# Kernel tuning notes

Hardware: AMD Instinct MI355X
Metric: run time of the kernel (lower is better)

The kernel has to match this reference:

```python
import jax, jax.numpy as jnp
import numpy as np

N = 50000   # nodes
E = 800000  # edges (avg degree 16)
G = 64      # graphs in batch

def _lin(k, fi, fo):
    kw, kb = jax.random.split(k)
    s = 1.0 / np.sqrt(fi)
    w = jax.random.uniform(kw, (fi, fo), minval=-s, maxval=s, dtype=jnp.float32)
    b = jax.random.uniform(kb, (fo,), minval=-s, maxval=s, dtype=jnp.float32)
    return w, b

def setup_inputs():
    key = jax.random.key(0)
    ks = jax.random.split(key, 12)
    pos = jax.random.normal(ks[0], (N, 3), dtype=jnp.float32)
    edge_index = jax.random.randint(ks[1], (2, E), 0, N, dtype=jnp.int32)
    batch = jnp.sort(jax.random.randint(ks[2], (N,), 0, G, dtype=jnp.int32))
    w_proj, b_proj = _lin(ks[3], 3, 64)
    # message passing layers: self-weight, neighbor-weight, bias
    ws0, bb0 = _lin(ks[4], 64, 64);  wn0, _ = _lin(jax.random.fold_in(ks[4], 1), 64, 64)
    ws1, bb1 = _lin(ks[5], 64, 64);  wn1, _ = _lin(jax.random.fold_in(ks[5], 1), 64, 64)
    ws2, bb2 = _lin(ks[6], 64, 128); wn2, _ = _lin(jax.random.fold_in(ks[6], 1), 64, 128)
    ws3, bb3 = _lin(ks[7], 256, 256); wn3, _ = _lin(jax.random.fold_in(ks[7], 1), 256, 256)
    # dense head: concat(max, mean) = 512 -> 512 -> 256
    wd1, bd1 = _lin(ks[8], 512, 512)
    wd2, bd2 = _lin(ks[9], 512, 256)
    return {"pos": pos, "edge_index": edge_index, "batch": batch,
            "w_proj": w_proj, "b_proj": b_proj,
            "ws0": ws0, "wn0": wn0, "bb0": bb0,
            "ws1": ws1, "wn1": wn1, "bb1": bb1,
            "ws2": ws2, "wn2": wn2, "bb2": bb2,
            "ws3": ws3, "wn3": wn3, "bb3": bb3,
            "wd1": wd1, "bd1": bd1, "wd2": wd2, "bd2": bd2}

def reference(pos, edge_index, batch, w_proj, b_proj,
              ws0, wn0, bb0, ws1, wn1, bb1, ws2, wn2, bb2, ws3, wn3, bb3,
              wd1, bd1, wd2, bd2):
    src, dst = edge_index[0], edge_index[1]
    x = pos @ w_proj + b_proj  # node projection [N,64]
    # in-degree counts, computed once
    deg = jnp.maximum(
        jax.ops.segment_sum(jnp.ones((E, 1), x.dtype), dst, num_segments=N), 1.0)

    def mp(h, ws, wn, b):
        # mean-aggregate neighbor messages: gather on src, scatter-add on dst
        agg = jax.ops.segment_sum(h[src], dst, num_segments=N) / deg
        return jax.nn.leaky_relu(h @ ws + agg @ wn + b)

    h0 = mp(x, ws0, wn0, bb0)   # [N,64]
    h1 = mp(h0, ws1, wn1, bb1)  # [N,64]
    h2 = mp(h1, ws2, wn2, bb2)  # [N,128]
    nf = mp(jnp.concatenate([h0, h1, h2], axis=-1), ws3, wn3, bb3)  # [N,256]

    # scatter max/mean pooling over graph ids
    gcnt = jnp.maximum(
        jax.ops.segment_sum(jnp.ones((N, 1), nf.dtype), batch, num_segments=G), 1.0)
    x1 = jax.ops.segment_max(nf, batch, num_segments=G)
    x2 = jax.ops.segment_sum(nf, batch, num_segments=G) / gcnt
    g = jnp.concatenate([x1, x2], axis=-1)  # [G,512]

    g = jax.nn.leaky_relu(g @ wd1 + bd1)
    return g @ wd2 + bd2  # [G,256]
```

## Files before the change

### kernel.cpp

```cpp
#include <hip/hip_runtime.h>
#include <math.h>

typedef _Float16 f16x8 __attribute__((ext_vector_type(8)));
typedef unsigned short us8 __attribute__((ext_vector_type(8)));
typedef float f32x4 __attribute__((ext_vector_type(4)));

__device__ inline unsigned short f2h(float f) {
    _Float16 h = (_Float16)f;
    return *(unsigned short*)&h;
}
__device__ inline float h2f(unsigned short u) {
    _Float16 h = *(_Float16*)&u;
    return (float)h;
}

__device__ __forceinline__ size_t pkoff(int row, int col, int KT) {
    return ((size_t)(row >> 4) * (KT >> 5) + (col >> 5)) * 512
         + (size_t)(((col >> 3) & 3) * 128 + ((row & 15) << 3) + (col & 7));
}

#define ECH 4096

__global__ __launch_bounds__(256)
void bucket_hist(const int* __restrict__ edst, int* __restrict__ bcnt, int E, int NB) {
    __shared__ int h[512];
    int tid = threadIdx.x;
    for (int i = tid; i < NB; i += 256) h[i] = 0;
    __syncthreads();
    int c0 = blockIdx.x * ECH, c1 = min(c0 + ECH, E);
    for (int e = c0 + tid; e < c1; e += 256) atomicAdd(&h[edst[e] >> 7], 1);
    __syncthreads();
    for (int i = tid; i < NB; i += 256) if (h[i]) atomicAdd(&bcnt[i], h[i]);
}

__global__ __launch_bounds__(512)
void bucket_scan(const int* __restrict__ bcnt, int* __restrict__ bbase,
                 int* __restrict__ bcur, int* __restrict__ rowstart, int NB, int n) {
    __shared__ int ws[8];
    int tid = threadIdx.x, lane = tid & 63, wid = tid >> 6;
    int v = (tid < NB) ? bcnt[tid] : 0;
    int x = v;
    for (int d = 1; d < 64; d <<= 1) { int y = __shfl_up(x, d); if (lane >= d) x += y; }
    if (lane == 63) ws[wid] = x;
    __syncthreads();
    int off = 0;
    for (int w = 0; w < wid; w++) off += ws[w];
    int excl = x - v + off;
    if (tid < NB) { bbase[tid] = excl; bcur[tid] = excl; }
    if (tid == 0) {
        int tot = 0;
        for (int w = 0; w < 8; w++) tot += ws[w];
        bbase[NB] = tot;
        rowstart[n] = tot;
    }
}

__global__ __launch_bounds__(256)
void bucket_scatter(const int* __restrict__ esrc_in, const int* __restrict__ edst_in,
                    int* __restrict__ bcur, unsigned* __restrict__ bedge, int E, int NB) {
    __shared__ int h[512];
    __shared__ int rb[512];
    int tid = threadIdx.x;
    for (int i = tid; i < NB; i += 256) h[i] = 0;
    __syncthreads();
    int c0 = blockIdx.x * ECH, c1 = min(c0 + ECH, E);
    for (int e = c0 + tid; e < c1; e += 256) atomicAdd(&h[edst_in[e] >> 7], 1);
    __syncthreads();
    for (int i = tid; i < NB; i += 256) {
        rb[i] = h[i] ? atomicAdd(&bcur[i], h[i]) : 0;
        h[i] = 0;
    }
    __syncthreads();
    for (int e = c0 + tid; e < c1; e += 256) {
        int dst = edst_in[e], src = esrc_in[e];
        int b = dst >> 7;
        int o = atomicAdd(&h[b], 1);
        bedge[rb[b] + o] = (unsigned)src | ((unsigned)(dst & 127) << 16);
    }
}

__global__ __launch_bounds__(256)
void node_csr(const unsigned* __restrict__ bedge, const int* __restrict__ bbase,
              int* __restrict__ rowstart, float* __restrict__ degf,
              unsigned short* __restrict__ esrc, int n) {
    __shared__ int cnt[128];
    __shared__ int cur[128];
    __shared__ int ws4[4];
    int b = blockIdx.x, tid = threadIdx.x;
    int lane = tid & 63, wid = tid >> 6;
    int n0 = b << 7;
    int eb0 = bbase[b], eb1 = bbase[b + 1];
    if (tid < 128) cnt[tid] = 0;
    __syncthreads();
    for (int e = eb0 + tid; e < eb1; e += 256) atomicAdd(&cnt[(bedge[e] >> 16) & 127], 1);
    __syncthreads();
    int v = (tid < 128) ? cnt[tid] : 0;
    int x = v;
    for (int d = 1; d < 64; d <<= 1) { int y = __shfl_up(x, d); if (lane >= d) x += y; }
    if (lane == 63) ws4[wid] = x;
    __syncthreads();
    int off = 0;
    for (int w = 0; w < wid; w++) off += ws4[w];
    int excl = x - v + off;
    if (tid < 128 && n0 + tid < n) {
        rowstart[n0 + tid] = eb0 + excl;
        cur[tid] = eb0 + excl;
        degf[n0 + tid] = (float)(v > 0 ? v : 1);
    }
    __syncthreads();
    for (int e = eb0 + tid; e < eb1; e += 256) {
        unsigned u = bedge[e];
        int p = atomicAdd(&cur[(u >> 16) & 127], 1);
        esrc[p] = (unsigned short)(u & 0xffffu);
    }
}

__global__ __launch_bounds__(256)
void prep_k(int* __restrict__ bcnt, float* __restrict__ pmax, float* __restrict__ psum, int G,
            const float* __restrict__ ws1, const float* __restrict__ wn1, unsigned short* __restrict__ WP1,
            const float* __restrict__ ws2, const float* __restrict__ wn2, unsigned short* __restrict__ WP2,
            const float* __restrict__ ws3, const float* __restrict__ wn3, unsigned short* __restrict__ WP3,
            const float* __restrict__ wp, const float* __restrict__ bp,
            const float* __restrict__ ws0, const float* __restrict__ wn0, const float* __restrict__ bb0,
            float* __restrict__ W0c, float* __restrict__ b0c,
            const float* __restrict__ pos, unsigned short* __restrict__ pos16, int N) {
    int t = blockIdx.x * 256 + threadIdx.x;
    if (t < 512) bcnt[t] = 0;
    if (t < G * 256) { pmax[t] = -INFINITY; psum[t] = 0.f; }
    if (t < 8192) {
        int k = t >> 6, n = t & 63;
        float v = (k < 64) ? ws1[k * 64 + n] : wn1[(k - 64) * 64 + n];
        WP1[pkoff(n, k, 128)] = f2h(v);
    }
    if (t < 16384) {
        int k = t >> 7, n = t & 127;
        float v = (k < 64) ? ws2[k * 128 + n] : wn2[(k - 64) * 128 + n];
        WP2[pkoff(n, k, 128)] = f2h(v);
    }
    if (t < 131072) {
        int k = t >> 8, n = t & 255;
        float v = (k < 256) ? ws3[k * 256 + n] : wn3[(k - 256) * 256 + n];
        WP3[pkoff(n, k, 512)] = f2h(v);
    }
    if (t < 384) {
        int j = t / 64, f = t & 63;
        const float* W = (j < 3) ? ws0 : wn0;
        int jj = (j < 3) ? j : j - 3;
        float acc = 0.f;
        for (int c = 0; c < 64; c++) acc += wp[jj * 64 + c] * W[c * 64 + f];
        W0c[j * 64 + f] = acc;
    }
    if (t < 64) {
        float acc = bb0[t];
        for (int c = 0; c < 64; c++) acc += bp[c] * (ws0[c * 64 + t] + wn0[c * 64 + t]);
        b0c[t] = acc;
    }
    if (t < 4 * N) {
        int n = t >> 2, j = t & 3;
        pos16[t] = (j < 3) ? f2h(pos[n * 3 + j]) : 0;
    }
}

__global__ __launch_bounds__(256)
void l0_k(const float* __restrict__ pos, const unsigned short* __restrict__ pos16,
          const float* __restrict__ W0c, const float* __restrict__ b0c,
          const int* __restrict__ rowstart, const unsigned short* __restrict__ esrc,
          const float* __restrict__ degf,
          unsigned short* __restrict__ XBrow, unsigned short* __restrict__ XBpk, int n_nodes) {
    int wave = threadIdx.x >> 6, lane = threadIdx.x & 63;
    int n = blockIdx.x * 4 + wave;
    if (n >= n_nodes) return;
    int e0 = rowstart[n], e1 = rowstart[n + 1];
    float ax = 0.f, ay = 0.f, az = 0.f;
    for (int e = e0 + lane; e < e1; e += 64) {
        int s = esrc[e];
        uint2 q = *(const uint2*)&pos16[(size_t)s * 4];
        ax += h2f((unsigned short)(q.x & 0xffffu));
        ay += h2f((unsigned short)(q.x >> 16));
        az += h2f((unsigned short)(q.y & 0xffffu));
    }
    #pragma unroll
    for (int d = 32; d; d >>= 1) {
        ax += __shfl_xor(ax, d);
        ay += __shfl_xor(ay, d);
        az += __shfl_xor(az, d);
    }
    float inv = 1.0f / degf[n];
    ax *= inv; ay *= inv; az *= inv;
    float px = pos[n * 3 + 0], py = pos[n * 3 + 1], pz = pos[n * 3 + 2];
    int f = lane;
    float v = b0c[f] + px * W0c[f] + py * W0c[64 + f] + pz * W0c[128 + f]
            + ax * W0c[192 + f] + ay * W0c[256 + f] + az * W0c[320 + f];
    v = (v > 0.f) ? v : 0.01f * v;
    unsigned short h = f2h(v);
    XBrow[(size_t)n * 256 + f] = h;
    XBpk[pkoff(n, f, 512)] = h;
}

template <int F, int KT>
__global__ __launch_bounds__(256)
void agg_pk(const unsigned short* __restrict__ src, int sstr,
            unsigned short* __restrict__ dpk, int dc,
            const int* __restrict__ rowstart, const unsigned short* __restrict__ esrc,
            const float* __restrict__ degf, int n_nodes) {
    int wave = threadIdx.x >> 6;
    int lane = threadIdx.x & 63;
    int n = blockIdx.x * 4 + wave;
    if (n >= n_nodes) return;
    const int ST = (F == 64) ? 2 : 1;
    int half = (F == 64) ? (lane >> 5) : 0;
    int li   = (F == 64) ? (lane & 31) : lane;
    int e0 = rowstart[n], e1 = rowstart[n + 1];
    float a0 = 0.f, a1 = 0.f;
    int e = e0 + half;
    for (; e + 7 * ST < e1; e += 8 * ST) {
        int s[8];
        unsigned p[8];
        #pragma unroll
        for (int j = 0; j < 8; j++) s[j] = esrc[e + j * ST];
        #pragma unroll
        for (int j = 0; j < 8; j++) p[j] = *(const unsigned*)&src[(size_t)s[j] * sstr + 2 * li];
        #pragma unroll
        for (int j = 0; j < 8; j++) {
            a0 += h2f((unsigned short)(p[j] & 0xffffu));
            a1 += h2f((unsigned short)(p[j] >> 16));
        }
    }
    for (; e + 3 * ST < e1; e += 4 * ST) {
        int s[4];
        unsigned p[4];
        #pragma unroll
        for (int j = 0; j < 4; j++) s[j] = esrc[e + j * ST];
        #pragma unroll
        for (int j = 0; j < 4; j++) p[j] = *(const unsigned*)&src[(size_t)s[j] * sstr + 2 * li];
        #pragma unroll
        for (int j = 0; j < 4; j++) {
            a0 += h2f((unsigned short)(p[j] & 0xffffu));
            a1 += h2f((unsigned short)(p[j] >> 16));
        }
    }
    for (; e < e1; e += ST) {
        int s = esrc[e];
        unsigned p = *(const unsigned*)&src[(size_t)s * sstr + 2 * li];
        a0 += h2f((unsigned short)(p & 0xffffu));
        a1 += h2f((unsigned short)(p >> 16));
    }
    if (F == 64) { a0 += __shfl_xor(a0, 32); a1 += __shfl_xor(a1, 32); }
    float inv = 1.0f / degf[n];
    unsigned out = (unsigned)f2h(a0 * inv) | ((unsigned)f2h(a1 * inv) << 16);
    if (F != 64 || lane < 32) {
        int c = dc + 2 * li;
        *(unsigned*)&dpk[pkoff(n, c, KT)] = out;
    }
}

__device__ inline void atomicMaxFloat(float* addr, float v) {
    if (v >= 0.f) atomicMax((int*)addr, __float_as_int(v));
    else          atomicMin((unsigned int*)addr, __float_as_uint(v));
}

template <int K, int KTA, int MT, int NTB, int POOL>
__global__ __launch_bounds__(256)
void gemm_fr(const unsigned short* __restrict__ Apk, int KA1, int ac1, int ac2,
             const unsigned short* __restrict__ Wpk, const float* __restrict__ bias,
             unsigned short* __restrict__ Drow, int dcol,
             unsigned short* __restrict__ Dpk, int KTD,
             float* __restrict__ pmax, float* __restrict__ psum,
             const int* __restrict__ batch, int M) {
    const int NS = K / 32;
    const int TROW = NTB * 16 + 8;
    const int TSZ = POOL ? 4 : (MT * 16) * TROW;
    __shared__ unsigned short tile_s[4][TSZ];
    int w = threadIdx.x >> 6;
    int lane = threadIdx.x & 63;
    int lm = lane & 15, kb = lane >> 4;
    int rb0 = (blockIdx.x * 4 + w) * MT;
    int nb0 = blockIdx.y * NTB;
    int m0 = rb0 * 16;
    if (m0 >= M) return;
    unsigned short* tile = tile_s[w];

    f32x4 acc[MT][NTB] = {};

    auto loadf = [&](f16x8* A_, f16x8* B_, int s) {
        int kk = s * 32;
        int phys = (kk < KA1) ? (ac1 + kk) : (ac2 + (kk - KA1));
        size_t ak = (size_t)(phys >> 5) * 512 + (size_t)lane * 8;
        #pragma unroll
        for (int mf = 0; mf < MT; mf++)
            A_[mf] = *(const f16x8*)&Apk[(size_t)(rb0 + mf) * (KTA / 32) * 512 + ak];
        #pragma unroll
        for (int nt = 0; nt < NTB; nt++)
            B_[nt] = *(const f16x8*)&Wpk[((size_t)(nb0 + nt) * (K / 32) + s) * 512 + (size_t)lane * 8];
    };
    auto domfma = [&](f16x8* A_, f16x8* B_) {
        #pragma unroll
        for (int nt = 0; nt < NTB; nt++)
            #pragma unroll
            for (int mf = 0; mf < MT; mf++)
                acc[mf][nt] = __builtin_amdgcn_mfma_f32_16x16x32_f16(A_[mf], B_[nt], acc[mf][nt], 0, 0, 0);
    };

    f16x8 aA[MT], bA[NTB], aB[MT], bB[NTB];
    loadf(aA, bA, 0);
    for (int s = 0; s < NS; s += 2) {
        loadf(aB, bB, s + 1);
        domfma(aA, bA);
        if (s + 2 < NS) loadf(aA, bA, s + 2);
        domfma(aB, bB);
    }

    if (!POOL) {
        #pragma unroll
        for (int nt = 0; nt < NTB; nt++) {
            int colL = nt * 16 + lm;
            float bv = bias[nb0 * 16 + colL];
            #pragma unroll
            for (int mf = 0; mf < MT; mf++) {
                #pragma unroll
                for (int r = 0; r < 4; r++) {
                    float v = acc[mf][nt][r] + bv;
                    v = (v > 0.f) ? v : 0.01f * v;
                    unsigned short h = f2h(v);
                    tile[(mf * 16 + kb * 4 + r) * TROW + colL] = h;
                    int gm = m0 + mf * 16 + kb * 4 + r;
                    if (gm < M) Drow[(size_t)gm * 256 + dcol + nb0 * 16 + colL] = h;
                }
            }
        }
        int dkg0 = (dcol + nb0 * 16) >> 5;
        #pragma unroll
        for (int mf = 0; mf < MT; mf++) {
            #pragma unroll
            for (int kg = 0; kg < NTB / 2; kg++) {
                us8 u = *(const us8*)&tile[(mf * 16 + lm) * TROW + kg * 32 + kb * 8];
                *(us8*)&Dpk[((size_t)(rb0 + mf) * (KTD / 32) + dkg0 + kg) * 512 + (size_t)lane * 8] = u;
            }
        }
    } else {
        int grow[MT * 4];
        #pragma unroll
        for (int mf = 0; mf < MT; mf++)
            #pragma unroll
            for (int r = 0; r < 4; r++) {
                int gm = m0 + mf * 16 + kb * 4 + r;
                grow[mf * 4 + r] = batch[gm < M ? gm : (M - 1)];
            }
        int mlast = m0 + MT * 16 - 1;
        bool uni = (batch[m0] == batch[mlast < M ? mlast : (M - 1)]);
        if (uni) {
            int g = grow[0];
            #pragma unroll
            for (int nt = 0; nt < NTB; nt++) {
                int col = (nb0 + nt) * 16 + lm;
                float bv = bias[col];
                float mx = -INFINITY, sm = 0.f;
                #pragma unroll
                for (int mf = 0; mf < MT; mf++) {
                    #pragma unroll
                    for (int r = 0; r < 4; r++) {
                        int gm = m0 + mf * 16 + kb * 4 + r;
                        if (gm >= M) continue;
                        float v = acc[mf][nt][r] + bv;
                        v = (v > 0.f) ? v : 0.01f * v;
                        mx = fmaxf(mx, v); sm += v;
                    }
                }
                mx = fmaxf(mx, __shfl_xor(mx, 16));
                mx = fmaxf(mx, __shfl_xor(mx, 32));
                sm += __shfl_xor(sm, 16);
                sm += __shfl_xor(sm, 32);
                if (kb == 0 && mx > -INFINITY) {
                    atomicMaxFloat(&pmax[g * 256 + col], mx);
                    atomicAdd(&psum[g * 256 + col], sm);
                }
            }
        } else {
            #pragma unroll
            for (int nt = 0; nt < NTB; nt++) {
                int col = (nb0 + nt) * 16 + lm;
                float bv = bias[col];
                int curg = -1; float mx = -INFINITY, sm = 0.f;
                #pragma unroll
                for (int mf = 0; mf < MT; mf++) {
                    #pragma unroll
                    for (int r = 0; r < 4; r++) {
                        int gm = m0 + mf * 16 + kb * 4 + r;
                        if (gm >= M) continue;
                        int g = grow[mf * 4 + r];
                        if (g != curg) {
                            if (curg >= 0) {
                                atomicMaxFloat(&pmax[curg * 256 + col], mx);
                                atomicAdd(&psum[curg * 256 + col], sm);
                            }
                            curg = g; mx = -INFINITY; sm = 0.f;
                        }
                        float v = acc[mf][nt][r] + bv;
                        v = (v > 0.f) ? v : 0.01f * v;
                        mx = fmaxf(mx, v); sm += v;
                    }
                }
                if (curg >= 0) {
                    atomicMaxFloat(&pmax[curg * 256 + col], mx);
                    atomicAdd(&psum[curg * 256 + col], sm);
                }
            }
        }
    }
}

template <int K, int FOUT>
__global__ __launch_bounds__(256)
void gemm_lrelu(const float* __restrict__ A1, int a1s, int a1c, int KA1,
                const float* __restrict__ A2, int a2s, int a2c,
                const float* __restrict__ W1, const float* __restrict__ W2,
                const float* __restrict__ bias,
                float* __restrict__ D, int dstr, int dcol, int M, int doRelu) {
    const int BM = 64, BN = 64, BK = 16;
    __shared__ float As[BK][BM];
    __shared__ float Bs[BK][BN];
    int tid = threadIdx.x;
    int m0 = blockIdx.x * BM;
    int n0 = blockIdx.y * BN;
    int tx = tid & 15;
    int ty = tid >> 4;
    float acc[4][4] = {};
    int mA = tid >> 2;
    int kA = (tid & 3) * 4;
    int kB = tid >> 4;
    int nB = (tid & 15) * 4;
    for (int k0 = 0; k0 < K; k0 += BK) {
        int kk = k0 + kA;
        const float* Ap; int Asr; int Acc;
        if (kk < KA1) { Ap = A1; Asr = a1s; Acc = a1c + kk; }
        else          { Ap = A2; Asr = a2s; Acc = a2c + (kk - KA1); }
        int gm = m0 + mA;
        float4 av;
        if (gm < M) av = *(const float4*)&Ap[(size_t)gm * Asr + Acc];
        else        av = float4{0.f, 0.f, 0.f, 0.f};
        As[kA + 0][mA] = av.x; As[kA + 1][mA] = av.y;
        As[kA + 2][mA] = av.z; As[kA + 3][mA] = av.w;
        int kw = k0 + kB;
        const float* Wp; int kwl;
        if (kw < K / 2) { Wp = W1; kwl = kw; } else { Wp = W2; kwl = kw - K / 2; }
        float4 bv = *(const float4*)&Wp[(size_t)kwl * FOUT + n0 + nB];
        *(float4*)&Bs[kB][nB] = bv;
        __syncthreads();
        #pragma unroll
        for (int k = 0; k < BK; k++) {
            float a[4], b[4];
            *(float4*)a = *(const float4*)&As[k][ty * 4];
            *(float4*)b = *(const float4*)&Bs[k][tx * 4];
            #pragma unroll
            for (int i = 0; i < 4; i++)
                #pragma unroll
                for (int j = 0; j < 4; j++)
                    acc[i][j] += a[i] * b[j];
        }
        __syncthreads();
    }
    #pragma unroll
    for (int i = 0; i < 4; i++) {
        int gm = m0 + ty * 4 + i;
        if (gm >= M) continue;
        #pragma unroll
        for (int j = 0; j < 4; j++) {
            int gn = n0 + tx * 4 + j;
            float v = acc[i][j] + bias[gn];
            if (doRelu) v = (v > 0.f) ? v : 0.01f * v;
            D[(size_t)gm * dstr + dcol + gn] = v;
        }
    }
}

__global__ __launch_bounds__(256)
void pool_final(const float* __restrict__ pmax, const float* __restrict__ psum,
                const int* __restrict__ batch, float* __restrict__ pooled,
                int G, int n_nodes) {
    int t = blockIdx.x * 256 + threadIdx.x;
    if (t >= G * 256) return;
    int g = t >> 8, f = t & 255;
    int lo = 0, hi = n_nodes;
    while (lo < hi) { int mid = (lo + hi) >> 1; if (batch[mid] < g) lo = mid + 1; else hi = mid; }
    int start = lo;
    lo = start; hi = n_nodes;
    while (lo < hi) { int mid = (lo + hi) >> 1; if (batch[mid] < g + 1) lo = mid + 1; else hi = mid; }
    int end = lo;
    int c = end - start;
    float mx = pmax[t];
    if (c == 0) mx = 0.f;
    pooled[g * 512 + f] = mx;
    pooled[g * 512 + 256 + f] = psum[t] / (float)(c > 0 ? c : 1);
}

extern "C" void kernel_launch(void* const* d_in, const int* in_sizes, int n_in,
                              void* d_out, int out_size, void* d_ws, size_t ws_size,
                              hipStream_t stream) {
    const float* pos   = (const float*)d_in[0];
    const int*   eidx  = (const int*)d_in[1];
    const int*   batch = (const int*)d_in[2];
    const float* w_proj = (const float*)d_in[3];
    const float* b_proj = (const float*)d_in[4];
    const float* ws0 = (const float*)d_in[5];  const float* wn0 = (const float*)d_in[6];  const float* bb0 = (const float*)d_in[7];
    const float* ws1 = (const float*)d_in[8];  const float* wn1 = (const float*)d_in[9];  const float* bb1 = (const float*)d_in[10];
    const float* ws2 = (const float*)d_in[11]; const float* wn2 = (const float*)d_in[12]; const float* bb2 = (const float*)d_in[13];
    const float* ws3 = (const float*)d_in[14]; const float* wn3 = (const float*)d_in[15]; const float* bb3 = (const float*)d_in[16];
    const float* wd1 = (const float*)d_in[17]; const float* bd1 = (const float*)d_in[18];
    const float* wd2 = (const float*)d_in[19]; const float* bd2 = (const float*)d_in[20];

    int N = in_sizes[0] / 3;
    int E = in_sizes[1] / 2;
    int G = out_size / 256;
    const int* esrc_in = eidx;
    const int* edst_in = eidx + E;

    int gbx1 = (N + 63) / 64;
    int gbx2 = (N + 127) / 128;
    int NRB = gbx1 * 4 + 8;
    int NB  = (N + 127) >> 7;

    char* base = (char*)d_ws;
    size_t off = 0;
    auto alloc = [&](size_t bytes) -> void* {
        void* p = base + off;
        off = (off + bytes + 255) & ~(size_t)255;
        return p;
    };
    int*   rowstart = (int*)alloc((size_t)(N + 1) * 4);
    float* degf     = (float*)alloc((size_t)N * 4);
    int*   bcnt     = (int*)alloc((size_t)512 * 4);
    int*   bbase    = (int*)alloc((size_t)513 * 4);
    int*   bcur     = (int*)alloc((size_t)512 * 4);
    unsigned* bedge = (unsigned*)alloc((size_t)E * 4);
    unsigned short* esrc = (unsigned short*)alloc((size_t)E * 2);
    unsigned short* pos16 = (unsigned short*)alloc((size_t)N * 4 * 2);
    float* W0c      = (float*)alloc((size_t)6 * 64 * 4);
    float* b0c      = (float*)alloc((size_t)64 * 4);
    unsigned short* XBrow  = (unsigned short*)alloc((size_t)N * 256 * 2);
    unsigned short* XBpk   = (unsigned short*)alloc((size_t)NRB * 16 * 512 * 2);
    float* pooled   = (float*)alloc((size_t)G * 512 * 4);
    float* hid      = (float*)alloc((size_t)G * 512 * 4);
    float* pmax     = (float*)alloc((size_t)G * 256 * 4);
    float* psum     = (float*)alloc((size_t)G * 256 * 4);
    unsigned short* WP1 = (unsigned short*)alloc((size_t)64 * 128 * 2);
    unsigned short* WP2 = (unsigned short*)alloc((size_t)128 * 128 * 2);
    unsigned short* WP3 = (unsigned short*)alloc((size_t)256 * 512 * 2);

    int prep_threads = 4 * N > 131072 ? 4 * N : 131072;
    prep_k<<<(prep_threads + 255) / 256, 256, 0, stream>>>(
        bcnt, pmax, psum, G,
        ws1, wn1, WP1, ws2, wn2, WP2, ws3, wn3, WP3,
        w_proj, b_proj, ws0, wn0, bb0, W0c, b0c, pos, pos16, N);

    int eb = (E + ECH - 1) / ECH;
    bucket_hist<<<eb, 256, 0, stream>>>(edst_in, bcnt, E, NB);
    bucket_scan<<<1, 512, 0, stream>>>(bcnt, bbase, bcur, rowstart, NB, N);
    bucket_scatter<<<eb, 256, 0, stream>>>(esrc_in, edst_in, bcur, bedge, E, NB);
    node_csr<<<NB, 256, 0, stream>>>(bedge, bbase, rowstart, degf, esrc, N);

    int ab = (N + 3) / 4;

    l0_k<<<ab, 256, 0, stream>>>(pos, pos16, W0c, b0c, rowstart, esrc, degf, XBrow, XBpk, N);

    agg_pk<64, 512><<<ab, 256, 0, stream>>>(XBrow, 256, XBpk, 256, rowstart, esrc, degf, N);
    gemm_fr<128, 512, 1, 4, 0><<<dim3(gbx1, 1), 256, 0, stream>>>(
        XBpk, 64, 0, 256, WP1, bb1, XBrow, 64, XBpk, 512, nullptr, nullptr, nullptr, N);

    agg_pk<64, 512><<<ab, 256, 0, stream>>>(XBrow + 64, 256, XBpk, 320, rowstart, esrc, degf, N);
    gemm_fr<128, 512, 1, 4, 0><<<dim3(gbx1, 2), 256, 0, stream>>>(
        XBpk, 64, 64, 320, WP2, bb2, XBrow, 128, XBpk, 512, nullptr, nullptr, nullptr, N);

    agg_pk<128, 512><<<ab, 256, 0, stream>>>(XBrow + 128, 256, XBpk, 384, rowstart, esrc, degf, N);
    gemm_fr<512, 512, 2, 8, 1><<<dim3(gbx2, 2), 256, 0, stream>>>(
        XBpk, 512, 0, 0, WP3, bb3, nullptr, 0, nullptr, 512, pmax, psum, batch, N);
    pool_final<<<(G * 256 + 255) / 256, 256, 0, stream>>>(pmax, psum, batch, pooled, G, N);

    gemm_lrelu<512, 512><<<dim3((G + 63) / 64, 8), 256, 0, stream>>>(
        pooled, 512, 0, 512, pooled, 512, 0, wd1, wd1 + 256 * 512, bd1, hid, 512, 0, G, 1);
    gemm_lrelu<512, 256><<<dim3((G + 63) / 64, 4), 256, 0, stream>>>(
        hid, 512, 0, 512, hid, 512, 0, wd2, wd2 + 256 * 256, bd2, (float*)d_out, 256, 0, G, 0);
}
```

Measured before the change: 281.6 us.

## Fuse neighbor aggregation and MFMA GEMM into one kernel for layers 1 and 2

Result: slower. 292.8 us (+4.0%).

```diff
diff --git a/kernel.cpp b/kernel.cpp
--- a/kernel.cpp
+++ b/kernel.cpp
@@ -195,6 +195,96 @@
     unsigned short h = f2h(v);
     XBrow[(size_t)n * 256 + f] = h;
     XBpk[pkoff(n, f, 512)] = h;
+}
+
+template <int FOUT>
+__global__ __launch_bounds__(256)
+void mp_k(const unsigned short* __restrict__ XBrow, int hc,
+          const unsigned short* __restrict__ Apk,
+          const unsigned short* __restrict__ Wpk, const float* __restrict__ bias,
+          const int* __restrict__ rowstart, const unsigned short* __restrict__ esrc,
+          const float* __restrict__ degf,
+          unsigned short* __restrict__ Drow, int dcol,
+          unsigned short* __restrict__ Dpk, int shc, int M) {
+    const int NTB = FOUT / 64;
+    __shared__ unsigned short Sh[2][64][8];
+    int w = threadIdx.x >> 6, lane = threadIdx.x & 63;
+    int lm = lane & 15, kb = lane >> 4;
+    int blk = blockIdx.x;
+    int m0 = blk * 16;
+    int half = lane >> 5, li = lane & 31;
+
+    #pragma unroll
+    for (int q = 0; q < 4; q++) {
+        int n = m0 + w * 4 + q;
+        int nc = (n < M) ? n : (M - 1);
+        int e0 = rowstart[nc], e1 = rowstart[nc + 1];
+        float a0 = 0.f, a1 = 0.f;
+        int e = e0 + half;
+        for (; e + 14 < e1; e += 16) {
+            int s[8]; unsigned p[8];
+            #pragma unroll
+            for (int j = 0; j < 8; j++) s[j] = esrc[e + j * 2];
+            #pragma unroll
+            for (int j = 0; j < 8; j++) p[j] = *(const unsigned*)&XBrow[(size_t)s[j] * 256 + hc + 2 * li];
+            #pragma unroll
+            for (int j = 0; j < 8; j++) {
+                a0 += h2f((unsigned short)(p[j] & 0xffffu));
+                a1 += h2f((unsigned short)(p[j] >> 16));
+            }
+        }
+        for (; e < e1; e += 2) {
+            int s = esrc[e];
+            unsigned p = *(const unsigned*)&XBrow[(size_t)s * 256 + hc + 2 * li];
+            a0 += h2f((unsigned short)(p & 0xffffu));
+            a1 += h2f((unsigned short)(p >> 16));
+        }
+        a0 += __shfl_xor(a0, 32);
+        a1 += __shfl_xor(a1, 32);
+        float inv = 1.0f / degf[nc];
+        unsigned outp = (unsigned)f2h(a0 * inv) | ((unsigned)f2h(a1 * inv) << 16);
+        if (lane < 32) {
+            int c = 2 * li;
+            int r = w * 4 + q;
+            *(unsigned*)&Sh[c >> 5][(((c >> 3) & 3) << 4) + r][c & 7] = outp;
+        }
+    }
+    __syncthreads();
+
+    if (threadIdx.x < 128) {
+        int ks = threadIdx.x >> 6, l = threadIdx.x & 63;
+        *(us8*)&Dpk[((size_t)blk * 16 + (shc >> 5) + ks) * 512 + (size_t)l * 8] =
+            *(const us8*)&Sh[ks][l][0];
+    }
+
+    f32x4 acc[NTB] = {};
+    #pragma unroll
+    for (int s = 0; s < 4; s++) {
+        f16x8 af;
+        if (s < 2)
+            af = *(const f16x8*)&Apk[((size_t)blk * 16 + ((hc + s * 32) >> 5)) * 512 + (size_t)lane * 8];
+        else
+            af = *(const f16x8*)&Sh[s - 2][lane][0];
+        #pragma unroll
+        for (int nt = 0; nt < NTB; nt++) {
+            f16x8 bf = *(const f16x8*)&Wpk[((size_t)(w * NTB + nt) * 4 + s) * 512 + (size_t)lane * 8];
+            acc[nt] = __builtin_amdgcn_mfma_f32_16x16x32_f16(af, bf, acc[nt], 0, 0, 0);
+        }
+    }
+    #pragma unroll
+    for (int nt = 0; nt < NTB; nt++) {
+        int colL = (w * NTB + nt) * 16 + lm;
+        float bv = bias[colL];
+        #pragma unroll
+        for (int r = 0; r < 4; r++) {
+            int gm = m0 + kb * 4 + r;
+            float v = acc[nt][r] + bv;
+            v = (v > 0.f) ? v : 0.01f * v;
+            unsigned short h = f2h(v);
+            if (gm < M) Drow[(size_t)gm * 256 + dcol + colL] = h;
+            Dpk[pkoff(gm, dcol + colL, 512)] = h;
+        }
+    }
 }
 
 template <int F, int KT>
@@ -514,9 +604,9 @@
     const int* esrc_in = eidx;
     const int* edst_in = eidx + E;
 
-    int gbx1 = (N + 63) / 64;
+    int mb16 = (N + 15) / 16;
     int gbx2 = (N + 127) / 128;
-    int NRB = gbx1 * 4 + 8;
+    int NRB = mb16 + 8;
     int NB  = (N + 127) >> 7;
 
     char* base = (char*)d_ws;
@@ -562,13 +652,11 @@
 
     l0_k<<<ab, 256, 0, stream>>>(pos, pos16, W0c, b0c, rowstart, esrc, degf, XBrow, XBpk, N);
 
-    agg_pk<64, 512><<<ab, 256, 0, stream>>>(XBrow, 256, XBpk, 256, rowstart, esrc, degf, N);
-    gemm_fr<128, 512, 1, 4, 0><<<dim3(gbx1, 1), 256, 0, stream>>>(
-        XBpk, 64, 0, 256, WP1, bb1, XBrow, 64, XBpk, 512, nullptr, nullptr, nullptr, N);
-
-    agg_pk<64, 512><<<ab, 256, 0, stream>>>(XBrow + 64, 256, XBpk, 320, rowstart, esrc, degf, N);
-    gemm_fr<128, 512, 1, 4, 0><<<dim3(gbx1, 2), 256, 0, stream>>>(
-        XBpk, 64, 64, 320, WP2, bb2, XBrow, 128, XBpk, 512, nullptr, nullptr, nullptr, N);
+    mp_k<64><<<mb16, 256, 0, stream>>>(
+        XBrow, 0, XBpk, WP1, bb1, rowstart, esrc, degf, XBrow, 64, XBpk, 256, N);
+
+    mp_k<128><<<mb16, 256, 0, stream>>>(
+        XBrow, 64, XBpk, WP2, bb2, rowstart, esrc, degf, XBrow, 128, XBpk, 320, N);
 
     agg_pk<128, 512><<<ab, 256, 0, stream>>>(XBrow + 128, 256, XBpk, 384, rowstart, esrc, degf, N);
     gemm_fr<512, 512, 2, 8, 1><<<dim3(gbx2, 2), 256, 0, stream>>>(
```
